# Kernel optimization log

Hardware: AMD Instinct MI355X
Metric: run time of the kernel (lower is better)

Reference implementation:

```python
import jax, jax.numpy as jnp
import numpy as np
from jax import lax

DIM = 512
IDIM = 1536
K = 7


def setup_inputs() -> dict:
    key = jax.random.key(0)
    ks = jax.random.split(key, 10)
    B, C, T = 16, DIM, 2048
    x = jax.random.normal(ks[0], (B, C, T), dtype=jnp.float32)
    dw_w = jax.random.normal(ks[1], (DIM, 1, K), dtype=jnp.float32) * (1.0 / np.sqrt(K))
    dw_b = jax.random.normal(ks[2], (DIM,), dtype=jnp.float32) * 0.01
    ln_g = jnp.ones((DIM,), dtype=jnp.float32)
    ln_b = jnp.zeros((DIM,), dtype=jnp.float32)
    w1 = jax.random.normal(ks[3], (IDIM, DIM), dtype=jnp.float32) * (1.0 / np.sqrt(DIM))
    b1 = jax.random.normal(ks[4], (IDIM,), dtype=jnp.float32) * 0.01
    grn_g = jax.random.normal(ks[5], (IDIM,), dtype=jnp.float32) * 0.02
    grn_b = jax.random.normal(ks[6], (IDIM,), dtype=jnp.float32) * 0.02
    w2 = jax.random.normal(ks[7], (DIM, IDIM), dtype=jnp.float32) * (1.0 / np.sqrt(IDIM))
    b2 = jax.random.normal(ks[8], (DIM,), dtype=jnp.float32) * 0.01
    return {"x": x, "dw_w": dw_w, "dw_b": dw_b, "ln_g": ln_g, "ln_b": ln_b,
            "w1": w1, "b1": b1, "grn_g": grn_g, "grn_b": grn_b, "w2": w2, "b2": b2}


def reference(x, dw_w, dw_b, ln_g, ln_b, w1, b1, grn_g, grn_b, w2, b2):
    residual = x  # [B, C, T]
    # depthwise conv1d, padding='same' style (K//2 each side)
    y = lax.conv_general_dilated(
        x, dw_w,
        window_strides=(1,),
        padding=[(K // 2, K // 2)],
        dimension_numbers=("NCH", "OIH", "NCH"),
        feature_group_count=DIM,
    ) + dw_b[None, :, None]
    y = jnp.transpose(y, (0, 2, 1))  # [B, T, C]
    # LayerNorm over channels, eps=1e-6
    mu = jnp.mean(y, axis=-1, keepdims=True)
    var = jnp.mean((y - mu) ** 2, axis=-1, keepdims=True)
    y = (y - mu) * lax.rsqrt(var + 1e-6) * ln_g + ln_b
    # pwconv1 + GELU (exact, erf-based as torch default)
    h = jnp.einsum("btc,ic->bti", y, w1) + b1  # [B, T, IDIM]
    h = jax.nn.gelu(h, approximate=False)
    # GRN: L2 norm over time axis (dim=1), mean over channels
    gx = jnp.sqrt(jnp.sum(h * h, axis=1, keepdims=True))  # [B, 1, IDIM]
    nx = gx / (jnp.mean(gx, axis=-1, keepdims=True) + 1e-6)
    h = grn_g * (h * nx) + grn_b + h
    # pwconv2
    y = jnp.einsum("bti,ci->btc", h, w2) + b2  # [B, T, C]
    y = jnp.transpose(y, (0, 2, 1))  # [B, C, T]
    return residual + y
```

## Files before the change

kernel.cpp:

```cpp
#include <hip/hip_runtime.h>
#include <math.h>

typedef unsigned short u16;
typedef unsigned int u32;
typedef __bf16 bf16x8_t __attribute__((ext_vector_type(8)));
typedef float f32x4_t __attribute__((ext_vector_type(4)));

__device__ __forceinline__ u16 f2bf(float f) {
  __bf16 b = (__bf16)f;
  return __builtin_bit_cast(u16, b);
}

__device__ __forceinline__ void gld16(const void* g, void* l) {
  __builtin_amdgcn_global_load_lds(
      (const __attribute__((address_space(1))) void*)g,
      (__attribute__((address_space(3))) void*)l, 16, 0, 0);
}

__device__ __forceinline__ float gelu_f(float v) {
  float z = 0.7978845608028654f * v * fmaf(0.044715f, v * v, 1.0f);
  float t = __builtin_amdgcn_exp2f(2.8853900817779268f * z);
  float r = __builtin_amdgcn_rcpf(t + 1.0f);
  return v - v * r;
}

__device__ __forceinline__ int swz8(int bid, int nwg) {
  int cpx = nwg >> 3;
  return (bid & 7) * cpx + (bid >> 3);
}

__global__ __launch_bounds__(256) void cast_kernel(const float* __restrict__ src,
                                                   u16* __restrict__ dst, int n) {
  int i = (blockIdx.x * 256 + threadIdx.x) * 4;
  if (i < n) {
    float4 v = *(const float4*)(src + i);
    uint2 o;
    o.x = (u32)f2bf(v.x) | ((u32)f2bf(v.y) << 16);
    o.y = (u32)f2bf(v.z) | ((u32)f2bf(v.w) << 16);
    *(uint2*)(dst + i) = o;
  }
}

__global__ __launch_bounds__(64) void b2ob_kernel(const float* __restrict__ w2,
                                                  const float* __restrict__ grn_b,
                                                  const float* __restrict__ b2,
                                                  float* __restrict__ out) {
  int c = blockIdx.x;
  int l = threadIdx.x;
  float p = 0.f;
  for (int i = l; i < 1536; i += 64) p += grn_b[i] * w2[(size_t)c * 1536 + i];
  #pragma unroll
  for (int s = 32; s; s >>= 1) p += __shfl_xor(p, s);
  if (l == 0) out[c] = b2[c] + p;
}

__global__ __launch_bounds__(512, 4) void conv_ln_kernel(const float* __restrict__ X,
                                                         const float* __restrict__ Wd,
                                                         const float* __restrict__ bd,
                                                         const float* __restrict__ lng,
                                                         const float* __restrict__ lnb,
                                                         u16* __restrict__ Y) {
  __shared__ float ystage[16 * 516];
  __shared__ float mu_s[16], rs_s[16];

  const int c = threadIdx.x;
  const int b = blockIdx.y;
  const int t0 = blockIdx.x * 64;

  const float* xr = X + ((size_t)b * 512 + c) * 2048;
  float wr[7];
  #pragma unroll
  for (int k = 0; k < 7; ++k) wr[k] = Wd[c * 7 + k];
  const float bdv = bd[c];
  const float lg = lng[c];
  const float lb = lnb[c];

  for (int ch = 0; ch < 4; ++ch) {
    const int tc0 = t0 + ch * 16;
    const int g = tc0 - 4;
    float w[24];
    if (g >= 0 && g + 24 <= 2048) {
      #pragma unroll
      for (int q = 0; q < 6; ++q) {
        float4 v = *(const float4*)(xr + g + q * 4);
        w[q * 4 + 0] = v.x; w[q * 4 + 1] = v.y;
        w[q * 4 + 2] = v.z; w[q * 4 + 3] = v.w;
      }
    } else {
      #pragma unroll
      for (int j = 0; j < 24; ++j) {
        int tt = g + j;
        w[j] = (tt >= 0 && tt < 2048) ? xr[tt] : 0.f;
      }
    }
    float outv[16];
    #pragma unroll
    for (int i = 0; i < 16; ++i) {
      float a = bdv;
      #pragma unroll
      for (int k = 0; k < 7; ++k) a = fmaf(w[i + 1 + k], wr[k], a);
      outv[i] = a;
      ystage[i * 516 + c] = a;
    }
    __syncthreads();
    {
      int r = c >> 5, cl = c & 31;
      float s = 0.f, q = 0.f;
      #pragma unroll
      for (int k = 0; k < 16; ++k) {
        float v = ystage[r * 516 + cl + k * 32];
        s += v; q += v * v;
      }
      #pragma unroll
      for (int m = 16; m; m >>= 1) { s += __shfl_xor(s, m); q += __shfl_xor(q, m); }
      if (cl == 0) {
        float mu = s * (1.f / 512.f);
        float var = q * (1.f / 512.f) - mu * mu;
        mu_s[r] = mu;
        rs_s[r] = rsqrtf(var + 1e-6f);
      }
    }
    __syncthreads();
    #pragma unroll
    for (int i = 0; i < 16; ++i) {
      float v = (outv[i] - mu_s[i]) * rs_s[i] * lg + lb;
      Y[(size_t)(b * 2048 + tc0 + i) * 512 + c] = f2bf(v);
    }
  }
}

__global__ __launch_bounds__(256) void grn_kernel(const float* __restrict__ gsum,
                                                  const float* __restrict__ grn_g,
                                                  float* __restrict__ svec) {
  __shared__ float red[256];
  int b = blockIdx.x, tid = threadIdx.x;
  float gx[6];
  float part = 0.f;
  #pragma unroll
  for (int it = 0; it < 6; ++it) {
    int i = it * 256 + tid;
    gx[it] = sqrtf(gsum[b * 1536 + i]);
    part += gx[it];
  }
  red[tid] = part;
  __syncthreads();
  for (int s = 128; s; s >>= 1) {
    if (tid < s) red[tid] += red[tid + s];
    __syncthreads();
  }
  float inv = 1.0f / (red[0] * (1.f / 1536.f) + 1e-6f);
  #pragma unroll
  for (int it = 0; it < 6; ++it) {
    int i = it * 256 + tid;
    svec[b * 1536 + i] = 1.0f + grn_g[i] * gx[it] * inv;
  }
}

__global__ __launch_bounds__(256) void w2s_kernel(const float* __restrict__ w2,
                                                  const float* __restrict__ svec,
                                                  u16* __restrict__ out) {
  size_t e0 = ((size_t)blockIdx.x * 256 + threadIdx.x) * 8;
  int i = (int)(e0 % 1536);
  size_t bc = e0 / 1536;
  int b = (int)(bc >> 9);
  size_t widx = (bc & 511) * 1536 + i;
  float4 wa = *(const float4*)(w2 + widx);
  float4 wb = *(const float4*)(w2 + widx + 4);
  float4 sa = *(const float4*)(svec + b * 1536 + i);
  float4 sb = *(const float4*)(svec + b * 1536 + i + 4);
  uint4 o;
  o.x = (u32)f2bf(wa.x * sa.x) | ((u32)f2bf(wa.y * sa.y) << 16);
  o.y = (u32)f2bf(wa.z * sa.z) | ((u32)f2bf(wa.w * sa.w) << 16);
  o.z = (u32)f2bf(wb.x * sb.x) | ((u32)f2bf(wb.y * sb.y) << 16);
  o.w = (u32)f2bf(wb.z * sb.z) | ((u32)f2bf(wb.w * sb.w) << 16);
  *(uint4*)(out + e0) = o;
}

template<int KD>
__device__ __forceinline__ void gemm_kloop(const u16* __restrict__ Ag,
                                           const u16* __restrict__ Bg,
                                           u16* lds, int NT,
                                           f32x4_t (&acc)[4][4]) {
  const int tid = threadIdx.x;
  const int l = tid & 63, l15 = l & 15, lq = l >> 4;
  const int w = tid >> 6;
  const int wm = w >> 1, wn = w & 1;
  const int rin = tid >> 3;
  const int cs = ((tid & 7) ^ (rin & 7)) << 3;
  u16* lA = lds;
  u16* lB = lds + 8192;

  for (int S = 0; S < NT; ++S) {
    const int kt = S * 64;
    #pragma unroll
    for (int c = 0; c < 4; ++c) {
      gld16(Ag + (size_t)(c * 32 + rin) * KD + kt + cs, lA + (c * 32 + w * 8) * 64);
      gld16(Bg + (size_t)(c * 32 + rin) * KD + kt + cs, lB + (c * 32 + w * 8) * 64);
    }
    __syncthreads();
    bf16x8_t af[4][2], bf[4][2];
    #pragma unroll
    for (int f = 0; f < 4; ++f) {
      const int Ra = wm * 64 + f * 16 + l15;
      const int Rb = wn * 64 + f * 16 + l15;
      #pragma unroll
      for (int kk = 0; kk < 2; ++kk) {
        af[f][kk] = *(const bf16x8_t*)(lA + Ra * 64 + (((kk * 4 + lq) ^ (Ra & 7)) << 3));
        bf[f][kk] = *(const bf16x8_t*)(lB + Rb * 64 + (((kk * 4 + lq) ^ (Rb & 7)) << 3));
      }
    }
    #pragma unroll
    for (int i = 0; i < 4; ++i)
      #pragma unroll
      for (int j = 0; j < 4; ++j)
        #pragma unroll
        for (int kk = 0; kk < 2; ++kk)
          acc[i][j] = __builtin_amdgcn_mfma_f32_16x16x32_bf16(af[i][kk], bf[j][kk], acc[i][j], 0, 0, 0);
    __syncthreads();
  }
}

__global__ __launch_bounds__(256) void gemm1_kernel(const u16* __restrict__ A,
                                                    const u16* __restrict__ Bw,
                                                    const float* __restrict__ b1,
                                                    u16* __restrict__ H,
                                                    float* __restrict__ gsum) {
  __shared__ __align__(16) u16 smem[16640];
  const int tid = threadIdx.x;
  const int l = tid & 63, l15 = l & 15, lq = l >> 4;
  const int w = tid >> 6, wm = w >> 1, wn = w & 1;
  const int wg = swz8(blockIdx.x, 3072);
  const int ntile = wg % 12, mtile = wg / 12;
  const int m0 = mtile * 128, n0 = ntile * 128;
  const int bidx = m0 >> 11;

  f32x4_t acc[4][4];
  #pragma unroll
  for (int i = 0; i < 4; ++i)
    #pragma unroll
    for (int j = 0; j < 4; ++j) {
      f32x4_t z = {0.f, 0.f, 0.f, 0.f};
      acc[i][j] = z;
    }

  gemm_kloop<512>(A + (size_t)m0 * 512, Bw + (size_t)n0 * 512, smem, 8, acc);

  float bj[4];
  #pragma unroll
  for (int nf = 0; nf < 4; ++nf) bj[nf] = b1[n0 + wn * 64 + nf * 16 + l15];

  float ss[4] = {0.f, 0.f, 0.f, 0.f};
  #pragma unroll
  for (int mf = 0; mf < 4; ++mf) {
    const int lr = wm * 64 + mf * 16 + lq * 4;
    #pragma unroll
    for (int nf = 0; nf < 4; ++nf) {
      const int cl = wn * 64 + nf * 16 + l15;
      #pragma unroll
      for (int r = 0; r < 4; ++r) {
        float g = gelu_f(acc[mf][nf][r] + bj[nf]);
        ss[nf] += g * g;
        smem[(lr + r) * 130 + cl] = f2bf(g);
      }
    }
  }
  #pragma unroll
  for (int nf = 0; nf < 4; ++nf) {
    float v = ss[nf];
    v += __shfl_xor(v, 16);
    v += __shfl_xor(v, 32);
    if (lq == 0) atomicAdd(&gsum[bidx * 1536 + n0 + wn * 64 + nf * 16 + l15], v);
  }
  __syncthreads();
  #pragma unroll
  for (int it = 0; it < 8; ++it) {
    int idx = it * 256 + tid;
    int row = idx >> 4, ch = idx & 15;
    uint4 v = *(const uint4*)(smem + row * 130 + ch * 8);
    *(uint4*)(H + (size_t)(m0 + row) * 1536 + n0 + ch * 8) = v;
  }
}

__global__ __launch_bounds__(256) void gemm2_kernel(const u16* __restrict__ Hm,
                                                    const u16* __restrict__ W2s,
                                                    const float* __restrict__ b2ob,
                                                    const float* __restrict__ X,
                                                    float* __restrict__ Out) {
  __shared__ __align__(16) u16 smem[16640];
  const int tid = threadIdx.x;
  const int l = tid & 63, l15 = l & 15, lq = l >> 4;
  const int w = tid >> 6, wm = w >> 1, wn = w & 1;
  const int wg = swz8(blockIdx.x, 1024);
  const int ntile = wg & 3, mtile = wg >> 2;
  const int m0 = mtile * 128, n0 = ntile * 128;
  const int bidx = m0 >> 11, t0 = m0 & 2047;

  f32x4_t acc[4][4];
  #pragma unroll
  for (int i = 0; i < 4; ++i)
    #pragma unroll
    for (int j = 0; j < 4; ++j) {
      f32x4_t z = {0.f, 0.f, 0.f, 0.f};
      acc[i][j] = z;
    }

  gemm_kloop<1536>(Hm + (size_t)m0 * 1536,
                   W2s + ((size_t)bidx * 512 + n0) * 1536, smem, 24, acc);

  float* st = (float*)smem;
  for (int half = 0; half < 2; ++half) {
    __syncthreads();
    if (wm == half) {
      #pragma unroll
      for (int mf = 0; mf < 4; ++mf) {
        const int lr = mf * 16 + lq * 4;
        #pragma unroll
        for (int nf = 0; nf < 4; ++nf) {
          const int cl = wn * 64 + nf * 16 + l15;
          #pragma unroll
          for (int r = 0; r < 4; ++r)
            st[(lr + r) * 129 + cl] = acc[mf][nf][r];
        }
      }
    }
    __syncthreads();
    const size_t obase = ((size_t)bidx * 512 + n0) * 2048 + (size_t)(t0 + half * 64 + l);
    #pragma unroll
    for (int cc = 0; cc < 32; ++cc) {
      const int c = w * 32 + cc;
      float v = st[l * 129 + c] + b2ob[n0 + c];
      size_t oi = obase + (size_t)c * 2048;
      Out[oi] = v + X[oi];
    }
  }
}

extern "C" void kernel_launch(void* const* d_in, const int* in_sizes, int n_in,
                              void* d_out, int out_size, void* d_ws, size_t ws_size,
                              hipStream_t stream) {
  const float* x     = (const float*)d_in[0];
  const float* dw_w  = (const float*)d_in[1];
  const float* dw_b  = (const float*)d_in[2];
  const float* ln_g  = (const float*)d_in[3];
  const float* ln_b  = (const float*)d_in[4];
  const float* w1    = (const float*)d_in[5];
  const float* b1    = (const float*)d_in[6];
  const float* grn_g = (const float*)d_in[7];
  const float* grn_b = (const float*)d_in[8];
  const float* w2    = (const float*)d_in[9];
  const float* b2    = (const float*)d_in[10];
  float* out = (float*)d_out;

  u16* y_ln = (u16*)d_ws;
  u16* w2s  = y_ln;
  u16* h    = y_ln + (size_t)32768 * 512;
  u16* w1b  = h + (size_t)32768 * 1536;
  float* gsum = (float*)(w1b + (size_t)1536 * 512);
  float* svec = gsum + 16 * 1536;
  float* b2ob = svec + 16 * 1536;

  hipMemsetAsync(gsum, 0, 16 * 1536 * sizeof(float), stream);
  cast_kernel<<<768, 256, 0, stream>>>(w1, w1b, 1536 * 512);
  b2ob_kernel<<<512, 64, 0, stream>>>(w2, grn_b, b2, b2ob);
  conv_ln_kernel<<<dim3(32, 16), 512, 0, stream>>>(x, dw_w, dw_b, ln_g, ln_b, y_ln);
  gemm1_kernel<<<3072, 256, 0, stream>>>(y_ln, w1b, b1, h, gsum);
  grn_kernel<<<16, 256, 0, stream>>>(gsum, grn_g, svec);
  w2s_kernel<<<6144, 256, 0, stream>>>(w2, svec, w2s);
  gemm2_kernel<<<1024, 256, 0, stream>>>(h, w2s, b2ob, x, out);
}
```

Baseline: 247.5 us.

## Double-buffer LDS tiles in GEMM k-loop to overlap loads with MFMA

The shared GEMM k-loop now ping-pongs between two LDS buffers. Each iteration issues the asynchronous global-to-LDS loads for the next k-tile before running the MFMA work on the current tile, so memory latency can hide behind compute. Both GEMM kernels switch to 64KB of dynamic shared memory to hold the two buffers. The larger LDS footprint per block lowers how many blocks fit on a CU, which cuts occupancy-based latency hiding.

```diff
diff --git a/kernel.cpp b/kernel.cpp
--- a/kernel.cpp
+++ b/kernel.cpp
@@ -187,17 +187,25 @@
   const int wm = w >> 1, wn = w & 1;
   const int rin = tid >> 3;
   const int cs = ((tid & 7) ^ (rin & 7)) << 3;
-  u16* lA = lds;
-  u16* lB = lds + 8192;
-
-  for (int S = 0; S < NT; ++S) {
-    const int kt = S * 64;
+
+  auto STAGE = [&](int buf, int kt) {
+    u16* lA = lds + buf * 16384;
+    u16* lB = lA + 8192;
     #pragma unroll
     for (int c = 0; c < 4; ++c) {
       gld16(Ag + (size_t)(c * 32 + rin) * KD + kt + cs, lA + (c * 32 + w * 8) * 64);
       gld16(Bg + (size_t)(c * 32 + rin) * KD + kt + cs, lB + (c * 32 + w * 8) * 64);
     }
-    __syncthreads();
+  };
+
+  STAGE(0, 0);
+  __syncthreads();
+
+  for (int S = 0; S < NT; ++S) {
+    const int cur = S & 1;
+    if (S + 1 < NT) STAGE(cur ^ 1, (S + 1) * 64);
+    u16* lA = lds + cur * 16384;
+    u16* lB = lA + 8192;
     bf16x8_t af[4][2], bf[4][2];
     #pragma unroll
     for (int f = 0; f < 4; ++f) {
@@ -225,7 +233,7 @@
                                                     const float* __restrict__ b1,
                                                     u16* __restrict__ H,
                                                     float* __restrict__ gsum) {
-  __shared__ __align__(16) u16 smem[16640];
+  extern __shared__ __align__(16) u16 lds[];
   const int tid = threadIdx.x;
   const int l = tid & 63, l15 = l & 15, lq = l >> 4;
   const int w = tid >> 6, wm = w >> 1, wn = w & 1;
@@ -243,7 +251,7 @@
       acc[i][j] = z;
     }
 
-  gemm_kloop<512>(A + (size_t)m0 * 512, Bw + (size_t)n0 * 512, smem, 8, acc);
+  gemm_kloop<512>(A + (size_t)m0 * 512, Bw + (size_t)n0 * 512, lds, 8, acc);
 
   float bj[4];
   #pragma unroll
@@ -260,7 +268,7 @@
       for (int r = 0; r < 4; ++r) {
         float g = gelu_f(acc[mf][nf][r] + bj[nf]);
         ss[nf] += g * g;
-        smem[(lr + r) * 130 + cl] = f2bf(g);
+        lds[(lr + r) * 130 + cl] = f2bf(g);
       }
     }
   }
@@ -276,7 +284,7 @@
   for (int it = 0; it < 8; ++it) {
     int idx = it * 256 + tid;
     int row = idx >> 4, ch = idx & 15;
-    uint4 v = *(const uint4*)(smem + row * 130 + ch * 8);
+    uint4 v = *(const uint4*)(lds + row * 130 + ch * 8);
     *(uint4*)(H + (size_t)(m0 + row) * 1536 + n0 + ch * 8) = v;
   }
 }
@@ -286,7 +294,7 @@
                                                     const float* __restrict__ b2ob,
                                                     const float* __restrict__ X,
                                                     float* __restrict__ Out) {
-  __shared__ __align__(16) u16 smem[16640];
+  extern __shared__ __align__(16) u16 lds[];
   const int tid = threadIdx.x;
   const int l = tid & 63, l15 = l & 15, lq = l >> 4;
   const int w = tid >> 6, wm = w >> 1, wn = w & 1;
@@ -305,9 +313,9 @@
     }
 
   gemm_kloop<1536>(Hm + (size_t)m0 * 1536,
-                   W2s + ((size_t)bidx * 512 + n0) * 1536, smem, 24, acc);
-
-  float* st = (float*)smem;
+                   W2s + ((size_t)bidx * 512 + n0) * 1536, lds, 24, acc);
+
+  float* st = (float*)lds;
   for (int half = 0; half < 2; ++half) {
     __syncthreads();
     if (wm == half) {
@@ -359,12 +367,17 @@
   float* svec = gsum + 16 * 1536;
   float* b2ob = svec + 16 * 1536;
 
+  (void)hipFuncSetAttribute((const void*)gemm1_kernel,
+                            hipFuncAttributeMaxDynamicSharedMemorySize, 65536);
+  (void)hipFuncSetAttribute((const void*)gemm2_kernel,
+                            hipFuncAttributeMaxDynamicSharedMemorySize, 65536);
+
   hipMemsetAsync(gsum, 0, 16 * 1536 * sizeof(float), stream);
   cast_kernel<<<768, 256, 0, stream>>>(w1, w1b, 1536 * 512);
   b2ob_kernel<<<512, 64, 0, stream>>>(w2, grn_b, b2, b2ob);
   conv_ln_kernel<<<dim3(32, 16), 512, 0, stream>>>(x, dw_w, dw_b, ln_g, ln_b, y_ln);
-  gemm1_kernel<<<3072, 256, 0, stream>>>(y_ln, w1b, b1, h, gsum);
+  gemm1_kernel<<<3072, 256, 65536, stream>>>(y_ln, w1b, b1, h, gsum);
   grn_kernel<<<16, 256, 0, stream>>>(gsum, grn_g, svec);
   w2s_kernel<<<6144, 256, 0, stream>>>(w2, svec, w2s);
-  gemm2_kernel<<<1024, 256, 0, stream>>>(h, w2s, b2ob, x, out);
-}
+  gemm2_kernel<<<1024, 256, 65536, stream>>>(h, w2s, b2ob, x, out);
+}
```

Measured after the change: 227.3 us. 1.09x faster.
